# Optimization experiments

Hardware: AMD Instinct MI355X
Metric: run time of the kernel (lower is better)

The kernel has to match this reference:

```python
import jax, jax.numpy as jnp
import numpy as np

BZ, C, H, W, M = 8, 64, 64, 64, 2048  # N = H*W = 4096 scene-graph nodes


def setup_inputs() -> dict:
    key = jax.random.key(0)
    k1, k2 = jax.random.split(key)
    sg_node_feats = jax.random.normal(k1, (BZ, C, H, W), dtype=jnp.float32)
    # weighted adjacency from SG nodes (N) to KG nodes (M)
    sg_kg_adj = jax.random.uniform(k2, (BZ, H * W, M), dtype=jnp.float32)
    return {"sg_node_feats": sg_node_feats, "sg_kg_adj": sg_kg_adj}


def reference(sg_node_feats, sg_kg_adj):
    bz, channels, height, width = sg_node_feats.shape
    x = sg_node_feats.reshape(bz, channels, height * width)  # (bz, C, N)
    degrees = sg_kg_adj.sum(axis=1)                          # (bz, M)
    norm = jnp.maximum(degrees, 1.0)                         # (bz, M)
    # broadcast-multiply + sum over N == batched GEMM (bz,C,N) x (bz,N,M)
    out = jnp.einsum('bcn,bnm->bcm', x, sg_kg_adj) / norm[:, None, :]
    return out.transpose(0, 2, 1)                            # (bz, M, C)
```

## Files before the change

kernel.cpp:

```cpp
#include <hip/hip_runtime.h>


typedef short bf16x8 __attribute__((ext_vector_type(8)));
typedef float f32x4 __attribute__((ext_vector_type(4)));

#define BZc 8
#define Cc 64
#define Nc 4096
#define Mc 2048
#define BMc 64
#define BKc 64
#define NSPLIT 2
#define NHALF (Nc / NSPLIT)
#define KITERS (NHALF / BKc)
#define SDW 36

#define PSUM_ELEMS (BZc * Mc * Cc)
#define PDEG_ELEMS (BZc * Mc)

__device__ __forceinline__ unsigned int pkbf(float a, float b) {
  unsigned int ua = __float_as_uint(a) + 0x8000u;
  unsigned int ub = __float_as_uint(b) + 0x8000u;
  return (ua >> 16) | (ub & 0xffff0000u);
}

__global__ __launch_bounds__(512, 4) void sgkg_kernel(
    const float* __restrict__ x,
    const float* __restrict__ adj,
    float* __restrict__ ws)
{
  __shared__ unsigned int adjT[BMc * SDW];
  __shared__ float degs[BMc];

  const int t = threadIdx.x;
  const int l = t & 63;
  const int w = t >> 6;

  const int bz     = blockIdx.x >> 6;
  const int m_base = ((blockIdx.x >> 1) & 31) * BMc;
  const int kh     = blockIdx.x & 1;

  const int mg  = ((w & 1) << 3) | (l & 7);
  const int p   = ((w >> 1) << 3) | (l >> 3);
  const int sm0 = mg << 2;

  const float* aptr =
      adj + (size_t)bz * Nc * Mc + (size_t)(kh * NHALF + 2 * p) * Mc + (m_base + sm0);
  const int wb = SDW * sm0 + ((((p >> 2) ^ (mg & 7))) << 2) + (p & 3);

  const int m_off = (w & 1) << 5;
  const int c_b   = (w >> 1) << 4;
  const int l15   = l & 15;
  const int l4    = l >> 4;

  const float* xb =
      x + ((size_t)bz * Cc + (c_b + l15)) * Nc + kh * NHALF + (l4 << 3);

  int aaddr[2][2];
#pragma unroll
  for (int tm = 0; tm < 2; ++tm) {
    const int m  = m_off + tm * 16 + l15;
    const int pi = (m >> 2) & 7;
    aaddr[tm][0] = SDW * m + (((l4) ^ pi) << 2);
    aaddr[tm][1] = SDW * m + (((4 + l4) ^ pi) << 2);
  }

  if (t < BMc) degs[t] = 0.0f;

  f32x4 acc0 = {0.f, 0.f, 0.f, 0.f};
  f32x4 acc1 = {0.f, 0.f, 0.f, 0.f};
  float dacc0 = 0.f, dacc1 = 0.f, dacc2 = 0.f, dacc3 = 0.f;

  float4 r0 = *(const float4*)aptr;
  float4 r1 = *(const float4*)(aptr + Mc);
  float4 xr0 = *(const float4*)(xb);
  float4 xr1 = *(const float4*)(xb + 4);
  float4 xr2 = *(const float4*)(xb + 32);
  float4 xr3 = *(const float4*)(xb + 36);

  for (int it = 0; it < KITERS; ++it) {
    __syncthreads();

    adjT[wb          ] = pkbf(r0.x, r1.x);
    adjT[wb +     SDW] = pkbf(r0.y, r1.y);
    adjT[wb + 2 * SDW] = pkbf(r0.z, r1.z);
    adjT[wb + 3 * SDW] = pkbf(r0.w, r1.w);

    dacc0 += r0.x + r1.x;
    dacc1 += r0.y + r1.y;
    dacc2 += r0.z + r1.z;
    dacc3 += r0.w + r1.w;

    const float* anext = (it + 1 < KITERS) ? (aptr + (size_t)BKc * Mc) : aptr;
    float4 s0 = *(const float4*)anext;
    float4 s1 = *(const float4*)(anext + Mc);

    const float* xnp = (it + 1 < KITERS) ? (xb + (it + 1) * BKc) : xb;
    float4 y0 = *(const float4*)(xnp);
    float4 y1 = *(const float4*)(xnp + 4);
    float4 y2 = *(const float4*)(xnp + 32);
    float4 y3 = *(const float4*)(xnp + 36);

    union { uint4 u; bf16x8 v; } B0, B1;
    B0.u = make_uint4(pkbf(xr0.x, xr0.y), pkbf(xr0.z, xr0.w),
                      pkbf(xr1.x, xr1.y), pkbf(xr1.z, xr1.w));
    B1.u = make_uint4(pkbf(xr2.x, xr2.y), pkbf(xr2.z, xr2.w),
                      pkbf(xr3.x, xr3.y), pkbf(xr3.z, xr3.w));

    __syncthreads();

    bf16x8 a00 = *(const bf16x8*)(adjT + aaddr[0][0]);
    bf16x8 a10 = *(const bf16x8*)(adjT + aaddr[1][0]);
    acc0 = __builtin_amdgcn_mfma_f32_16x16x32_bf16(a00, B0.v, acc0, 0, 0, 0);
    acc1 = __builtin_amdgcn_mfma_f32_16x16x32_bf16(a10, B0.v, acc1, 0, 0, 0);
    bf16x8 a01 = *(const bf16x8*)(adjT + aaddr[0][1]);
    bf16x8 a11 = *(const bf16x8*)(adjT + aaddr[1][1]);
    acc0 = __builtin_amdgcn_mfma_f32_16x16x32_bf16(a01, B1.v, acc0, 0, 0, 0);
    acc1 = __builtin_amdgcn_mfma_f32_16x16x32_bf16(a11, B1.v, acc1, 0, 0, 0);

    aptr = anext;
    r0 = s0; r1 = s1;
    xr0 = y0; xr1 = y1; xr2 = y2; xr3 = y3;
  }

  __syncthreads();
  atomicAdd(&degs[sm0 + 0], dacc0);
  atomicAdd(&degs[sm0 + 1], dacc1);
  atomicAdd(&degs[sm0 + 2], dacc2);
  atomicAdd(&degs[sm0 + 3], dacc3);

  float* psum = ws + (size_t)kh * PSUM_ELEMS;
#pragma unroll
  for (int tm = 0; tm < 2; ++tm) {
    const f32x4 acc = tm ? acc1 : acc0;
#pragma unroll
    for (int r = 0; r < 4; ++r) {
      const int ml   = m_off + tm * 16 + (l4 << 2) + r;
      const size_t o = ((size_t)(bz * Mc + m_base + ml)) * Cc + (c_b + l15);
      psum[o] = acc[r];
    }
  }

  __syncthreads();
  if (t < BMc) {
    float* pdeg = ws + 2 * (size_t)PSUM_ELEMS + (size_t)kh * PDEG_ELEMS;
    pdeg[bz * Mc + m_base + t] = degs[t];
  }
}

__global__ __launch_bounds__(256) void norm_kernel(
    const float* __restrict__ ws, float* __restrict__ out)
{
  const int i = blockIdx.x * 256 + threadIdx.x;
  const float4* p0 = (const float4*)ws;
  const float4* p1 = (const float4*)(ws + PSUM_ELEMS);
  const float* d0  = ws + 2 * (size_t)PSUM_ELEMS;
  const float* d1  = d0 + PDEG_ELEMS;

  const int bm = i >> 4;
  const float den = fmaxf(d0[bm] + d1[bm], 1.0f);

  float4 a = p0[i];
  float4 b = p1[i];
  float4 r;
  r.x = (a.x + b.x) / den;
  r.y = (a.y + b.y) / den;
  r.z = (a.z + b.z) / den;
  r.w = (a.w + b.w) / den;
  ((float4*)out)[i] = r;
}

extern "C" void kernel_launch(void* const* d_in, const int* in_sizes, int n_in,
                              void* d_out, int out_size, void* d_ws, size_t ws_size,
                              hipStream_t stream) {
  const float* x   = (const float*)d_in[0];
  const float* adj = (const float*)d_in[1];
  float* out       = (float*)d_out;
  float* ws        = (float*)d_ws;
  (void)in_sizes; (void)n_in; (void)out_size; (void)ws_size;

  sgkg_kernel<<<dim3(BZc * (Mc / BMc) * NSPLIT), dim3(512), 0, stream>>>(x, adj, ws);
  norm_kernel<<<dim3(PSUM_ELEMS / 4 / 256), dim3(256), 0, stream>>>(ws, out);
}
```

Baseline: 384.9 us.

## Widen M tile to 128, split N four ways, give each wave a 32x32 output tile

Doubles the M tile to 128 so one block stages two adjacency panels, and raises the N split from 2 to 4 so the grid keeps the same block count. Each wave now computes a 32x32 output tile with four MFMAs per k-step, reusing A fragments across two channel tiles. The x software prefetch is dropped in favour of loads issued at the top of each iteration. Four partial-sum buffers double the workspace traffic and the norm kernel now reads four partials, adding memory traffic in exchange for more MFMA reuse.

Measured after the change: 378.8 us. No clear change (-1.6%).

```diff
diff --git a/kernel.cpp b/kernel.cpp
--- a/kernel.cpp
+++ b/kernel.cpp
@@ -8,12 +8,13 @@
 #define Cc 64
 #define Nc 4096
 #define Mc 2048
-#define BMc 64
+#define BMc 128
 #define BKc 64
-#define NSPLIT 2
-#define NHALF (Nc / NSPLIT)
-#define KITERS (NHALF / BKc)
+#define NSPLIT 4
+#define NSEG (Nc / NSPLIT)
+#define KITERS (NSEG / BKc)
 #define SDW 36
+#define PANEL (64 * SDW)
 
 #define PSUM_ELEMS (BZc * Mc * Cc)
 #define PDEG_ELEMS (BZc * Mc)
@@ -29,7 +30,7 @@
     const float* __restrict__ adj,
     float* __restrict__ ws)
 {
-  __shared__ unsigned int adjT[BMc * SDW];
+  __shared__ unsigned int adjT[2 * PANEL];
   __shared__ float degs[BMc];
 
   const int t = threadIdx.x;
@@ -37,113 +38,141 @@
   const int w = t >> 6;
 
   const int bz     = blockIdx.x >> 6;
-  const int m_base = ((blockIdx.x >> 1) & 31) * BMc;
-  const int kh     = blockIdx.x & 1;
+  const int mb     = (blockIdx.x >> 2) & 15;
+  const int kh     = blockIdx.x & 3;
+  const int m_base = mb * BMc;
 
   const int mg  = ((w & 1) << 3) | (l & 7);
   const int p   = ((w >> 1) << 3) | (l >> 3);
   const int sm0 = mg << 2;
 
   const float* aptr =
-      adj + (size_t)bz * Nc * Mc + (size_t)(kh * NHALF + 2 * p) * Mc + (m_base + sm0);
-  const int wb = SDW * sm0 + ((((p >> 2) ^ (mg & 7))) << 2) + (p & 3);
-
-  const int m_off = (w & 1) << 5;
-  const int c_b   = (w >> 1) << 4;
+      adj + (size_t)bz * Nc * Mc + (size_t)(kh * NSEG + 2 * p) * Mc + (m_base + sm0);
+  const int wb = SDW * sm0 + (((p >> 2) ^ (mg & 7)) << 2) + (p & 3);
+
+  const int m_off = (w & 3) << 5;
+  const int c_b   = (w >> 2) << 5;
   const int l15   = l & 15;
   const int l4    = l >> 4;
 
   const float* xb =
-      x + ((size_t)bz * Cc + (c_b + l15)) * Nc + kh * NHALF + (l4 << 3);
+      x + ((size_t)bz * Cc + (c_b + l15)) * Nc + kh * NSEG + (l4 << 3);
 
   int aaddr[2][2];
 #pragma unroll
   for (int tm = 0; tm < 2; ++tm) {
     const int m  = m_off + tm * 16 + l15;
-    const int pi = (m >> 2) & 7;
-    aaddr[tm][0] = SDW * m + (((l4) ^ pi) << 2);
-    aaddr[tm][1] = SDW * m + (((4 + l4) ^ pi) << 2);
+    const int q  = m >> 6;
+    const int ml = m & 63;
+    const int pi = (ml >> 2) & 7;
+    aaddr[tm][0] = q * PANEL + SDW * ml + ((l4 ^ pi) << 2);
+    aaddr[tm][1] = q * PANEL + SDW * ml + (((4 + l4) ^ pi) << 2);
   }
 
   if (t < BMc) degs[t] = 0.0f;
 
-  f32x4 acc0 = {0.f, 0.f, 0.f, 0.f};
-  f32x4 acc1 = {0.f, 0.f, 0.f, 0.f};
-  float dacc0 = 0.f, dacc1 = 0.f, dacc2 = 0.f, dacc3 = 0.f;
-
-  float4 r0 = *(const float4*)aptr;
-  float4 r1 = *(const float4*)(aptr + Mc);
-  float4 xr0 = *(const float4*)(xb);
-  float4 xr1 = *(const float4*)(xb + 4);
-  float4 xr2 = *(const float4*)(xb + 32);
-  float4 xr3 = *(const float4*)(xb + 36);
+  f32x4 acc00 = {0.f,0.f,0.f,0.f}, acc01 = {0.f,0.f,0.f,0.f};
+  f32x4 acc10 = {0.f,0.f,0.f,0.f}, acc11 = {0.f,0.f,0.f,0.f};
+  float da00=0.f, da01=0.f, da02=0.f, da03=0.f;
+  float da10=0.f, da11=0.f, da12=0.f, da13=0.f;
+
+  float4 r00 = *(const float4*)(aptr);
+  float4 r01 = *(const float4*)(aptr + Mc);
+  float4 r10 = *(const float4*)(aptr + 64);
+  float4 r11 = *(const float4*)(aptr + 64 + Mc);
 
   for (int it = 0; it < KITERS; ++it) {
+    const float* xit0 = xb + it * BKc;
+    const float* xit1 = xit0 + 16 * Nc;
+    float4 x00 = *(const float4*)(xit0);
+    float4 x01 = *(const float4*)(xit0 + 4);
+    float4 x02 = *(const float4*)(xit0 + 32);
+    float4 x03 = *(const float4*)(xit0 + 36);
+    float4 x10 = *(const float4*)(xit1);
+    float4 x11 = *(const float4*)(xit1 + 4);
+    float4 x12 = *(const float4*)(xit1 + 32);
+    float4 x13 = *(const float4*)(xit1 + 36);
+
     __syncthreads();
 
-    adjT[wb          ] = pkbf(r0.x, r1.x);
-    adjT[wb +     SDW] = pkbf(r0.y, r1.y);
-    adjT[wb + 2 * SDW] = pkbf(r0.z, r1.z);
-    adjT[wb + 3 * SDW] = pkbf(r0.w, r1.w);
-
-    dacc0 += r0.x + r1.x;
-    dacc1 += r0.y + r1.y;
-    dacc2 += r0.z + r1.z;
-    dacc3 += r0.w + r1.w;
+    adjT[wb          ]         = pkbf(r00.x, r01.x);
+    adjT[wb +     SDW]         = pkbf(r00.y, r01.y);
+    adjT[wb + 2 * SDW]         = pkbf(r00.z, r01.z);
+    adjT[wb + 3 * SDW]         = pkbf(r00.w, r01.w);
+    adjT[PANEL + wb          ] = pkbf(r10.x, r11.x);
+    adjT[PANEL + wb +     SDW] = pkbf(r10.y, r11.y);
+    adjT[PANEL + wb + 2 * SDW] = pkbf(r10.z, r11.z);
+    adjT[PANEL + wb + 3 * SDW] = pkbf(r10.w, r11.w);
+
+    da00 += r00.x + r01.x;  da01 += r00.y + r01.y;
+    da02 += r00.z + r01.z;  da03 += r00.w + r01.w;
+    da10 += r10.x + r11.x;  da11 += r10.y + r11.y;
+    da12 += r10.z + r11.z;  da13 += r10.w + r11.w;
 
     const float* anext = (it + 1 < KITERS) ? (aptr + (size_t)BKc * Mc) : aptr;
-    float4 s0 = *(const float4*)anext;
-    float4 s1 = *(const float4*)(anext + Mc);
-
-    const float* xnp = (it + 1 < KITERS) ? (xb + (it + 1) * BKc) : xb;
-    float4 y0 = *(const float4*)(xnp);
-    float4 y1 = *(const float4*)(xnp + 4);
-    float4 y2 = *(const float4*)(xnp + 32);
-    float4 y3 = *(const float4*)(xnp + 36);
-
-    union { uint4 u; bf16x8 v; } B0, B1;
-    B0.u = make_uint4(pkbf(xr0.x, xr0.y), pkbf(xr0.z, xr0.w),
-                      pkbf(xr1.x, xr1.y), pkbf(xr1.z, xr1.w));
-    B1.u = make_uint4(pkbf(xr2.x, xr2.y), pkbf(xr2.z, xr2.w),
-                      pkbf(xr3.x, xr3.y), pkbf(xr3.z, xr3.w));
+    float4 s00 = *(const float4*)(anext);
+    float4 s01 = *(const float4*)(anext + Mc);
+    float4 s10 = *(const float4*)(anext + 64);
+    float4 s11 = *(const float4*)(anext + 64 + Mc);
+
+    union { uint4 u; bf16x8 v; } B00, B01, B10, B11;
+    B00.u = make_uint4(pkbf(x00.x, x00.y), pkbf(x00.z, x00.w),
+                       pkbf(x01.x, x01.y), pkbf(x01.z, x01.w));
+    B01.u = make_uint4(pkbf(x02.x, x02.y), pkbf(x02.z, x02.w),
+                       pkbf(x03.x, x03.y), pkbf(x03.z, x03.w));
+    B10.u = make_uint4(pkbf(x10.x, x10.y), pkbf(x10.z, x10.w),
+                       pkbf(x11.x, x11.y), pkbf(x11.z, x11.w));
+    B11.u = make_uint4(pkbf(x12.x, x12.y), pkbf(x12.z, x12.w),
+                       pkbf(x13.x, x13.y), pkbf(x13.z, x13.w));
 
     __syncthreads();
 
     bf16x8 a00 = *(const bf16x8*)(adjT + aaddr[0][0]);
     bf16x8 a10 = *(const bf16x8*)(adjT + aaddr[1][0]);
-    acc0 = __builtin_amdgcn_mfma_f32_16x16x32_bf16(a00, B0.v, acc0, 0, 0, 0);
-    acc1 = __builtin_amdgcn_mfma_f32_16x16x32_bf16(a10, B0.v, acc1, 0, 0, 0);
+    acc00 = __builtin_amdgcn_mfma_f32_16x16x32_bf16(a00, B00.v, acc00, 0, 0, 0);
+    acc01 = __builtin_amdgcn_mfma_f32_16x16x32_bf16(a00, B10.v, acc01, 0, 0, 0);
+    acc10 = __builtin_amdgcn_mfma_f32_16x16x32_bf16(a10, B00.v, acc10, 0, 0, 0);
+    acc11 = __builtin_amdgcn_mfma_f32_16x16x32_bf16(a10, B10.v, acc11, 0, 0, 0);
     bf16x8 a01 = *(const bf16x8*)(adjT + aaddr[0][1]);
     bf16x8 a11 = *(const bf16x8*)(adjT + aaddr[1][1]);
-    acc0 = __builtin_amdgcn_mfma_f32_16x16x32_bf16(a01, B1.v, acc0, 0, 0, 0);
-    acc1 = __builtin_amdgcn_mfma_f32_16x16x32_bf16(a11, B1.v, acc1, 0, 0, 0);
+    acc00 = __builtin_amdgcn_mfma_f32_16x16x32_bf16(a01, B01.v, acc00, 0, 0, 0);
+    acc01 = __builtin_amdgcn_mfma_f32_16x16x32_bf16(a01, B11.v, acc01, 0, 0, 0);
+    acc10 = __builtin_amdgcn_mfma_f32_16x16x32_bf16(a11, B01.v, acc10, 0, 0, 0);
+    acc11 = __builtin_amdgcn_mfma_f32_16x16x32_bf16(a11, B11.v, acc11, 0, 0, 0);
 
     aptr = anext;
-    r0 = s0; r1 = s1;
-    xr0 = y0; xr1 = y1; xr2 = y2; xr3 = y3;
+    r00 = s00; r01 = s01; r10 = s10; r11 = s11;
   }
 
   __syncthreads();
-  atomicAdd(&degs[sm0 + 0], dacc0);
-  atomicAdd(&degs[sm0 + 1], dacc1);
-  atomicAdd(&degs[sm0 + 2], dacc2);
-  atomicAdd(&degs[sm0 + 3], dacc3);
+  atomicAdd(&degs[     sm0 + 0], da00);
+  atomicAdd(&degs[     sm0 + 1], da01);
+  atomicAdd(&degs[     sm0 + 2], da02);
+  atomicAdd(&degs[     sm0 + 3], da03);
+  atomicAdd(&degs[64 + sm0 + 0], da10);
+  atomicAdd(&degs[64 + sm0 + 1], da11);
+  atomicAdd(&degs[64 + sm0 + 2], da12);
+  atomicAdd(&degs[64 + sm0 + 3], da13);
 
   float* psum = ws + (size_t)kh * PSUM_ELEMS;
 #pragma unroll
   for (int tm = 0; tm < 2; ++tm) {
-    const f32x4 acc = tm ? acc1 : acc0;
-#pragma unroll
-    for (int r = 0; r < 4; ++r) {
-      const int ml   = m_off + tm * 16 + (l4 << 2) + r;
-      const size_t o = ((size_t)(bz * Mc + m_base + ml)) * Cc + (c_b + l15);
-      psum[o] = acc[r];
+#pragma unroll
+    for (int ct = 0; ct < 2; ++ct) {
+      const f32x4 acc = tm ? (ct ? acc11 : acc10) : (ct ? acc01 : acc00);
+#pragma unroll
+      for (int r = 0; r < 4; ++r) {
+        const int ml   = m_off + tm * 16 + (l4 << 2) + r;
+        const int c    = c_b + ct * 16 + l15;
+        const size_t o = ((size_t)(bz * Mc + m_base + ml)) * Cc + c;
+        psum[o] = acc[r];
+      }
     }
   }
 
   __syncthreads();
   if (t < BMc) {
-    float* pdeg = ws + 2 * (size_t)PSUM_ELEMS + (size_t)kh * PDEG_ELEMS;
+    float* pdeg = ws + (size_t)NSPLIT * PSUM_ELEMS + (size_t)kh * PDEG_ELEMS;
     pdeg[bz * Mc + m_base + t] = degs[t];
   }
 }
@@ -152,21 +181,25 @@
     const float* __restrict__ ws, float* __restrict__ out)
 {
   const int i = blockIdx.x * 256 + threadIdx.x;
-  const float4* p0 = (const float4*)ws;
-  const float4* p1 = (const float4*)(ws + PSUM_ELEMS);
-  const float* d0  = ws + 2 * (size_t)PSUM_ELEMS;
-  const float* d1  = d0 + PDEG_ELEMS;
+  const float4* p0 = (const float4*)(ws);
+  const float4* p1 = (const float4*)(ws + (size_t)1 * PSUM_ELEMS);
+  const float4* p2 = (const float4*)(ws + (size_t)2 * PSUM_ELEMS);
+  const float4* p3 = (const float4*)(ws + (size_t)3 * PSUM_ELEMS);
+  const float* dg  = ws + (size_t)NSPLIT * PSUM_ELEMS;
 
   const int bm = i >> 4;
-  const float den = fmaxf(d0[bm] + d1[bm], 1.0f);
+  const float den = fmaxf(dg[bm] + dg[PDEG_ELEMS + bm] +
+                          dg[2 * PDEG_ELEMS + bm] + dg[3 * PDEG_ELEMS + bm], 1.0f);
 
   float4 a = p0[i];
   float4 b = p1[i];
+  float4 c = p2[i];
+  float4 d = p3[i];
   float4 r;
-  r.x = (a.x + b.x) / den;
-  r.y = (a.y + b.y) / den;
-  r.z = (a.z + b.z) / den;
-  r.w = (a.w + b.w) / den;
+  r.x = (a.x + b.x + c.x + d.x) / den;
+  r.y = (a.y + b.y + c.y + d.y) / den;
+  r.z = (a.z + b.z + c.z + d.z) / den;
+  r.w = (a.w + b.w + c.w + d.w) / den;
   ((float4*)out)[i] = r;
 }
 
```
